# Optimization experiments

Hardware: AMD Instinct MI355X
Metric: run time of the kernel (lower is better)

The kernel has to match this reference:

```python
import jax, jax.numpy as jnp
import numpy as np

B, T, C = 4, 2048, 1024
H = 16
D = C // H  # head_dim = 64


def setup_inputs() -> dict:
    key = jax.random.key(0)
    k1, k2, k3 = jax.random.split(key, 3)
    x = jax.random.normal(k1, (B, T, C), dtype=jnp.float32)
    # torch Linear weights are [out_features, in_features]; scale like default init
    W_qkv = jax.random.normal(k2, (3 * C, C), dtype=jnp.float32) * (1.0 / np.sqrt(C))
    W_proj = jax.random.normal(k3, (C, C), dtype=jnp.float32) * (1.0 / np.sqrt(C))
    return {"x": x, "W_qkv": W_qkv, "W_proj": W_proj}


def reference(x, W_qkv, W_proj):
    # qkv projection: x @ W_qkv.T -> (B,T,3C), split into q,k,v
    qkv = jnp.einsum('btc,oc->bto', x, W_qkv)
    q, k, v = jnp.split(qkv, 3, axis=-1)
    # reshape to (B,H,T,D)
    q = q.reshape(B, T, H, D).transpose(0, 2, 1, 3)
    k = k.reshape(B, T, H, D).transpose(0, 2, 1, 3)
    v = v.reshape(B, T, H, D).transpose(0, 2, 1, 3)
    scale = jnp.sqrt(jnp.float32(D))
    # explicit (B,H,T,T) scores, as in the original module
    attn = jnp.einsum('bhqd,bhkd->bhqk', q, k) / scale
    causal = jnp.tril(jnp.ones((T, T), dtype=bool))
    attn = jnp.where(causal, attn, -jnp.inf)
    attn = jax.nn.softmax(attn, axis=-1)
    out = jnp.einsum('bhqk,bhkd->bhqd', attn, v)
    out = out.transpose(0, 2, 1, 3).reshape(B, T, C)
    return jnp.einsum('btc,oc->bto', out, W_proj)
```

## Files before the change

### kernel.cpp

```cpp
#include <hip/hip_runtime.h>

typedef __attribute__((ext_vector_type(8))) short short8;
typedef __attribute__((ext_vector_type(4))) float f32x4;
typedef __attribute__((ext_vector_type(16))) float f32x16;
typedef __attribute__((ext_vector_type(4))) unsigned int u32x4;

#define AS1(p) ((const __attribute__((address_space(1))) void*)(p))
#define AS3(p) ((__attribute__((address_space(3))) void*)(p))

#define B_ 4
#define T_ 2048
#define C_ 1024
#define H_ 16
#define D_ 64
#define M_ (B_*T_)

__device__ __forceinline__ unsigned short f2bf(float f) {
  union { float f; unsigned u; } v; v.f = f;
  return (unsigned short)((v.u + 0x7fffu + ((v.u >> 16) & 1u)) >> 16);
}

__device__ __forceinline__ unsigned cvt_pk_bf16(float lo, float hi2) {
  unsigned r;
  asm("v_cvt_pk_bf16_f32 %0, %1, %2" : "=v"(r) : "v"(lo), "v"(hi2));
  return r;
}

__global__ void cast_f32_bf16(const float* __restrict__ in, unsigned short* __restrict__ out, int n) {
  int i = (blockIdx.x * blockDim.x + threadIdx.x) * 4;
  int stride = gridDim.x * blockDim.x * 4;
  for (; i < n; i += stride) {
    float4 f = *reinterpret_cast<const float4*>(in + i);
    ushort4 o;
    o.x = f2bf(f.x); o.y = f2bf(f.y); o.z = f2bf(f.z); o.w = f2bf(f.w);
    *reinterpret_cast<ushort4*>(out + i) = o;
  }
}

template<int EPI>
__global__ __launch_bounds__(256) void gemm_bt(
    const unsigned short* __restrict__ A, const unsigned short* __restrict__ Bt,
    float* __restrict__ Cout, int M, int N, int K,
    unsigned short* __restrict__ qb, unsigned short* __restrict__ kb,
    unsigned short* __restrict__ vtb) {
  __shared__ unsigned short As[128 * 32];
  __shared__ unsigned short Bs[128 * 32];
  const int tid = threadIdx.x;
  const int lane = tid & 63;
  const int w = tid >> 6;
  const int wr = w >> 1, wc = w & 1;
  const int lr = lane & 15, lg = lane >> 4;
  const int ntiles = N >> 7;
  const int mt = blockIdx.x / ntiles, nt = blockIdx.x % ntiles;
  const int m0 = mt << 7, n0 = nt << 7;

  f32x4 acc[4][4];
  #pragma unroll
  for (int i = 0; i < 4; i++)
    #pragma unroll
    for (int j = 0; j < 4; j++) acc[i][j] = (f32x4){0.f, 0.f, 0.f, 0.f};

  const int wbase = tid & ~63;
  for (int k0 = 0; k0 < K; k0 += 32) {
    #pragma unroll
    for (int t = 0; t < 2; t++) {
      int slot = t * 256 + tid;
      int row = slot >> 2, kg = slot & 3;
      const unsigned short* ga = A + (size_t)(m0 + row) * K + k0 + kg * 8;
      char* la = (char*)As + (size_t)(t * 256 + wbase) * 16;
      __builtin_amdgcn_global_load_lds(AS1(ga), AS3(la), 16, 0, 0);
      const unsigned short* gb = Bt + (size_t)(n0 + row) * K + k0 + kg * 8;
      char* lb = (char*)Bs + (size_t)(t * 256 + wbase) * 16;
      __builtin_amdgcn_global_load_lds(AS1(gb), AS3(lb), 16, 0, 0);
    }
    __syncthreads();
    short8 af[4], bf[4];
    #pragma unroll
    for (int i = 0; i < 4; i++) {
      af[i] = *reinterpret_cast<const short8*>(&As[(wr * 64 + i * 16 + lr) * 32 + lg * 8]);
      bf[i] = *reinterpret_cast<const short8*>(&Bs[(wc * 64 + i * 16 + lr) * 32 + lg * 8]);
    }
    #pragma unroll
    for (int i = 0; i < 4; i++)
      #pragma unroll
      for (int j = 0; j < 4; j++)
        acc[i][j] = __builtin_amdgcn_mfma_f32_16x16x32_bf16(af[i], bf[j], acc[i][j], 0, 0, 0);
    __syncthreads();
  }

  #pragma unroll
  for (int i = 0; i < 4; i++) {
    #pragma unroll
    for (int j = 0; j < 4; j++) {
      #pragma unroll
      for (int r = 0; r < 4; r++) {
        int row = m0 + wr * 64 + i * 16 + lg * 4 + r;
        int col = n0 + wc * 64 + j * 16 + lr;
        float v = acc[i][j][r];
        if (EPI == 0) {
          Cout[(size_t)row * N + col] = v;
        } else {
          int which = col >> 10;
          int c = col & 1023;
          int h = c >> 6, d = c & 63;
          int b = row >> 11, t2 = row & 2047;
          if (which == 0) {
            qb[(((size_t)(b * H_ + h)) * T_ + t2) * D_ + d] = f2bf(v * 0.125f);
          } else if (which == 1) {
            kb[(((size_t)(b * H_ + h)) * T_ + t2) * D_ + d] = f2bf(v);
          } else {
            vtb[(((size_t)(b * H_ + h)) * D_ + d) * T_ + t2] = f2bf(v);
          }
        }
      }
    }
  }
}

__global__ __launch_bounds__(256, 2) void attn_fwd(
    const unsigned short* __restrict__ qb, const unsigned short* __restrict__ kb,
    const unsigned short* __restrict__ vtb, unsigned short* __restrict__ ob) {
  __shared__ unsigned short Kl[2 * 64 * 64];
  const int tid = threadIdx.x;
  const int lane = tid & 63;
  const int w = tid >> 6;
  const int q31 = lane & 31;
  const int hi = lane >> 5;

  const int bid = blockIdx.x;
  const int bh = (bid & 7) * 8 + ((bid >> 3) & 7);
  const int qt = 15 - (bid >> 6);
  const int qb0 = qt << 7;
  const int b = bh >> 4, h = bh & 15;

  const unsigned short* Q  = qb  + (size_t)bh * T_ * D_;
  const unsigned short* Kp = kb  + (size_t)bh * T_ * D_;
  const unsigned short* Vt = vtb + (size_t)bh * D_ * T_;

  const int qlo = qb0 + w * 32;
  const int qg = qlo + q31;
  const int qmax = qlo + 31;

  short8 qf[4];
  #pragma unroll
  for (int ch = 0; ch < 4; ch++)
    qf[ch] = *reinterpret_cast<const short8*>(Q + (size_t)qg * D_ + ch * 16 + hi * 8);

  f32x16 acc0, acc1;
  #pragma unroll
  for (int r = 0; r < 16; r++) { acc0[r] = 0.f; acc1[r] = 0.f; }
  float mrun = -INFINITY, lrun = 0.f;

  auto stage = [&](int buf, int k0) {
    #pragma unroll
    for (int sh = 0; sh < 2; sh++) {
      int s = sh * 256 + tid;
      int row = s >> 3;
      int xlin = (s & 7) * 16;
      int src = xlin ^ ((row & 7) << 4);
      const unsigned short* g = Kp + (size_t)(k0 + row) * D_ + (src >> 1);
      char* l = (char*)Kl + buf * 8192 + (size_t)(sh * 256 + (tid & ~63)) * 16;
      __builtin_amdgcn_global_load_lds(AS1(g), AS3(l), 16, 0, 0);
    }
  };

  const int nt = qb0 / 64 + 2;
  stage(0, 0);
  __syncthreads();

  for (int t = 0; t < nt; t++) {
    const int k0 = t * 64;
    if (t + 1 < nt) stage((t + 1) & 1, k0 + 64);

    if (k0 <= qmax) {
      const char* kbase = (const char*)Kl + (t & 1) * 8192;

      f32x16 s0, s1;
      #pragma unroll
      for (int r = 0; r < 16; r++) { s0[r] = 0.f; s1[r] = 0.f; }
      __builtin_amdgcn_s_setprio(1);
      #pragma unroll
      for (int kc = 0; kc < 2; kc++) {
        const int row = kc * 32 + q31;
        const int sw = (row & 7) << 4;
        #pragma unroll
        for (int ch = 0; ch < 4; ch++) {
          const int cb = ch * 32 + hi * 16;
          short8 kf = *reinterpret_cast<const short8*>(kbase + row * 128 + (cb ^ sw));
          if (kc == 0) s0 = __builtin_amdgcn_mfma_f32_32x32x16_bf16(kf, qf[ch], s0, 0, 0, 0);
          else         s1 = __builtin_amdgcn_mfma_f32_32x32x16_bf16(kf, qf[ch], s1, 0, 0, 0);
        }
      }
      __builtin_amdgcn_s_setprio(0);

      if (k0 + 63 > qlo) {
        #pragma unroll
        for (int r = 0; r < 16; r++) {
          const int kl = (r & 3) + 8 * (r >> 2) + 4 * hi;
          if (k0 + kl > qg)      s0[r] = -INFINITY;
          if (k0 + 32 + kl > qg) s1[r] = -INFINITY;
        }
      }

      float tm[8];
      #pragma unroll
      for (int r = 0; r < 8; r++)
        tm[r] = fmaxf(fmaxf(s0[r], s0[r + 8]), fmaxf(s1[r], s1[r + 8]));
      #pragma unroll
      for (int off = 4; off > 0; off >>= 1)
        #pragma unroll
        for (int r = 0; r < off; r++) tm[r] = fmaxf(tm[r], tm[r + off]);
      float pmax = fmaxf(tm[0], __shfl_xor(tm[0], 32));

      if (!__all(pmax - mrun <= 8.0f)) {
        const float mnew = fmaxf(mrun, pmax);
        const float alpha = __expf(mrun - mnew);
        lrun *= alpha;
        #pragma unroll
        for (int r = 0; r < 16; r++) { acc0[r] *= alpha; acc1[r] *= alpha; }
        mrun = mnew;
      }

      #pragma unroll
      for (int r = 0; r < 16; r++) { s0[r] = __expf(s0[r] - mrun); s1[r] = __expf(s1[r] - mrun); }
      float ts[8];
      #pragma unroll
      for (int r = 0; r < 8; r++)
        ts[r] = (s0[r] + s0[r + 8]) + (s1[r] + s1[r + 8]);
      #pragma unroll
      for (int off = 4; off > 0; off >>= 1)
        #pragma unroll
        for (int r = 0; r < off; r++) ts[r] += ts[r + off];
      lrun += ts[0] + __shfl_xor(ts[0], 32);

      #pragma unroll
      for (int kc = 0; kc < 2; kc++) {
        unsigned w8[8], rw8[8];
        #pragma unroll
        for (int j = 0; j < 8; j++) {
          float a = (kc == 0) ? s0[2 * j] : s1[2 * j];
          float bb = (kc == 0) ? s0[2 * j + 1] : s1[2 * j + 1];
          w8[j] = cvt_pk_bf16(a, bb);
        }
        #pragma unroll
        for (int j = 0; j < 8; j++) rw8[j] = (unsigned)__shfl_xor((int)w8[j], 32);

        __builtin_amdgcn_s_setprio(1);
        #pragma unroll
        for (int ks = 0; ks < 2; ks++) {
          unsigned a0 = hi ? rw8[4 * ks + 2] : w8[4 * ks + 0];
          unsigned a1 = hi ? rw8[4 * ks + 3] : w8[4 * ks + 1];
          unsigned a2 = hi ? w8[4 * ks + 2]  : rw8[4 * ks + 0];
          unsigned a3 = hi ? w8[4 * ks + 3]  : rw8[4 * ks + 1];
          u32x4 pw = {a0, a1, a2, a3};
          union { u32x4 u; short8 s; } cv; cv.u = pw;
          const int kb2 = k0 + kc * 32 + ks * 16;
          #pragma unroll
          for (int ds = 0; ds < 2; ds++) {
            short8 vf = *reinterpret_cast<const short8*>(
                Vt + (size_t)(ds * 32 + q31) * T_ + kb2 + hi * 8);
            if (ds == 0) acc0 = __builtin_amdgcn_mfma_f32_32x32x16_bf16(vf, cv.s, acc0, 0, 0, 0);
            else         acc1 = __builtin_amdgcn_mfma_f32_32x32x16_bf16(vf, cv.s, acc1, 0, 0, 0);
          }
        }
        __builtin_amdgcn_s_setprio(0);
      }
    }
    __syncthreads();
  }

  const float inv = 1.f / lrun;
  unsigned short* orow = ob + ((size_t)(b * T_ + qg)) * C_ + h * D_;
  #pragma unroll
  for (int ds = 0; ds < 2; ds++) {
    #pragma unroll
    for (int g = 0; g < 4; g++) {
      ushort4 o4;
      if (ds == 0) {
        o4.x = f2bf(acc0[4 * g + 0] * inv); o4.y = f2bf(acc0[4 * g + 1] * inv);
        o4.z = f2bf(acc0[4 * g + 2] * inv); o4.w = f2bf(acc0[4 * g + 3] * inv);
      } else {
        o4.x = f2bf(acc1[4 * g + 0] * inv); o4.y = f2bf(acc1[4 * g + 1] * inv);
        o4.z = f2bf(acc1[4 * g + 2] * inv); o4.w = f2bf(acc1[4 * g + 3] * inv);
      }
      *reinterpret_cast<ushort4*>(orow + ds * 32 + 8 * g + 4 * hi) = o4;
    }
  }
}

extern "C" void kernel_launch(void* const* d_in, const int* in_sizes, int n_in,
                              void* d_out, int out_size, void* d_ws, size_t ws_size,
                              hipStream_t stream) {
  const float* x = (const float*)d_in[0];
  const float* W_qkv = (const float*)d_in[1];
  const float* W_proj = (const float*)d_in[2];
  float* out = (float*)d_out;

  char* ws = (char*)d_ws;
  unsigned short* xb     = (unsigned short*)(ws);
  unsigned short* wqkvb  = (unsigned short*)(ws + 16777216);
  unsigned short* wprojb = (unsigned short*)(ws + 23068672);
  unsigned short* qb     = (unsigned short*)(ws + 25165824);
  unsigned short* kb     = (unsigned short*)(ws + 41943040);
  unsigned short* vtb    = (unsigned short*)(ws + 58720256);
  unsigned short* ob     = xb;

  const int nx = M_ * C_;
  const int nwqkv = 3 * C_ * C_;
  const int nwproj = C_ * C_;

  cast_f32_bf16<<<2048, 256, 0, stream>>>(x, xb, nx);
  cast_f32_bf16<<<2048, 256, 0, stream>>>(W_qkv, wqkvb, nwqkv);
  cast_f32_bf16<<<1024, 256, 0, stream>>>(W_proj, wprojb, nwproj);

  gemm_bt<1><<<(M_ / 128) * (3 * C_ / 128), 256, 0, stream>>>(
      xb, wqkvb, nullptr, M_, 3 * C_, C_, qb, kb, vtb);

  attn_fwd<<<B_ * H_ * (T_ / 128), 256, 0, stream>>>(qb, kb, vtb, ob);

  gemm_bt<0><<<(M_ / 128) * (C_ / 128), 256, 0, stream>>>(
      ob, wprojb, out, M_, C_, C_, nullptr, nullptr, nullptr);
}
```

Before: 241.2 us.

## Split KV range across waves with LDS merge of partial softmax states

Each block now handles 32 queries, and its four waves process interleaved KV tiles in parallel. Each wave loads K directly from global memory into registers instead of staging it through double-buffered LDS. Per-wave partial accumulators, max and sum are then combined through LDS in a tree merge. This is meant to improve parallelism and load balance and to remove the per-tile barriers. In exchange it gives up K reuse across waves, which raises global/L2 traffic and adds merge overhead.

```diff
diff --git a/kernel.cpp b/kernel.cpp
--- a/kernel.cpp
+++ b/kernel.cpp
@@ -120,7 +120,7 @@
 __global__ __launch_bounds__(256, 2) void attn_fwd(
     const unsigned short* __restrict__ qb, const unsigned short* __restrict__ kb,
     const unsigned short* __restrict__ vtb, unsigned short* __restrict__ ob) {
-  __shared__ unsigned short Kl[2 * 64 * 64];
+  __shared__ float Ml[2][64][34];
   const int tid = threadIdx.x;
   const int lane = tid & 63;
   const int w = tid >> 6;
@@ -129,161 +129,177 @@
 
   const int bid = blockIdx.x;
   const int bh = (bid & 7) * 8 + ((bid >> 3) & 7);
-  const int qt = 15 - (bid >> 6);
-  const int qb0 = qt << 7;
+  const int qu = 63 - (bid >> 6);
+  const int qb0 = qu << 5;
   const int b = bh >> 4, h = bh & 15;
 
   const unsigned short* Q  = qb  + (size_t)bh * T_ * D_;
   const unsigned short* Kp = kb  + (size_t)bh * T_ * D_;
   const unsigned short* Vt = vtb + (size_t)bh * D_ * T_;
 
-  const int qlo = qb0 + w * 32;
-  const int qg = qlo + q31;
-  const int qmax = qlo + 31;
+  const int qg = qb0 + q31;
 
   short8 qf[4];
   #pragma unroll
   for (int ch = 0; ch < 4; ch++)
-    qf[ch] = *reinterpret_cast<const short8*>(Q + (size_t)qg * D_ + ch * 16 + hi * 8);
+    qf[ch] = *reinterpret_cast<const short8*>(Q + qg * D_ + ch * 16 + hi * 8);
 
   f32x16 acc0, acc1;
   #pragma unroll
   for (int r = 0; r < 16; r++) { acc0[r] = 0.f; acc1[r] = 0.f; }
   float mrun = -INFINITY, lrun = 0.f;
 
-  auto stage = [&](int buf, int k0) {
-    #pragma unroll
-    for (int sh = 0; sh < 2; sh++) {
-      int s = sh * 256 + tid;
-      int row = s >> 3;
-      int xlin = (s & 7) * 16;
-      int src = xlin ^ ((row & 7) << 4);
-      const unsigned short* g = Kp + (size_t)(k0 + row) * D_ + (src >> 1);
-      char* l = (char*)Kl + buf * 8192 + (size_t)(sh * 256 + (tid & ~63)) * 16;
-      __builtin_amdgcn_global_load_lds(AS1(g), AS3(l), 16, 0, 0);
-    }
+  const int ntk = (qb0 >> 6) + 1;
+
+  for (int t = w; t < ntk; t += 4) {
+    const int k0 = t << 6;
+
+    short8 kf0[4], kf1[4];
+    #pragma unroll
+    for (int ch = 0; ch < 4; ch++)
+      kf0[ch] = *reinterpret_cast<const short8*>(Kp + (k0 + q31) * D_ + ch * 16 + hi * 8);
+    #pragma unroll
+    for (int ch = 0; ch < 4; ch++)
+      kf1[ch] = *reinterpret_cast<const short8*>(Kp + (k0 + 32 + q31) * D_ + ch * 16 + hi * 8);
+
+    f32x16 s0, s1;
+    #pragma unroll
+    for (int r = 0; r < 16; r++) { s0[r] = 0.f; s1[r] = 0.f; }
+    __builtin_amdgcn_s_setprio(1);
+    #pragma unroll
+    for (int ch = 0; ch < 4; ch++)
+      s0 = __builtin_amdgcn_mfma_f32_32x32x16_bf16(kf0[ch], qf[ch], s0, 0, 0, 0);
+    #pragma unroll
+    for (int ch = 0; ch < 4; ch++)
+      s1 = __builtin_amdgcn_mfma_f32_32x32x16_bf16(kf1[ch], qf[ch], s1, 0, 0, 0);
+    __builtin_amdgcn_s_setprio(0);
+
+    if (t == ntk - 1) {
+      #pragma unroll
+      for (int r = 0; r < 16; r++) {
+        const int kl = (r & 3) + 8 * (r >> 2) + 4 * hi;
+        if (k0 + kl > qg)      s0[r] = -INFINITY;
+        if (k0 + 32 + kl > qg) s1[r] = -INFINITY;
+      }
+    }
+
+    float tm[8];
+    #pragma unroll
+    for (int r = 0; r < 8; r++)
+      tm[r] = fmaxf(fmaxf(s0[r], s0[r + 8]), fmaxf(s1[r], s1[r + 8]));
+    #pragma unroll
+    for (int off = 4; off > 0; off >>= 1)
+      #pragma unroll
+      for (int r = 0; r < off; r++) tm[r] = fmaxf(tm[r], tm[r + off]);
+    float pmax = fmaxf(tm[0], __shfl_xor(tm[0], 32));
+
+    if (!__all(pmax - mrun <= 8.0f)) {
+      const float mnew = fmaxf(mrun, pmax);
+      const float alpha = __expf(mrun - mnew);
+      lrun *= alpha;
+      #pragma unroll
+      for (int r = 0; r < 16; r++) { acc0[r] *= alpha; acc1[r] *= alpha; }
+      mrun = mnew;
+    }
+
+    #pragma unroll
+    for (int r = 0; r < 16; r++) { s0[r] = __expf(s0[r] - mrun); s1[r] = __expf(s1[r] - mrun); }
+    float ts[8];
+    #pragma unroll
+    for (int r = 0; r < 8; r++)
+      ts[r] = (s0[r] + s0[r + 8]) + (s1[r] + s1[r + 8]);
+    #pragma unroll
+    for (int off = 4; off > 0; off >>= 1)
+      #pragma unroll
+      for (int r = 0; r < off; r++) ts[r] += ts[r + off];
+    lrun += ts[0] + __shfl_xor(ts[0], 32);
+
+    #pragma unroll
+    for (int kc = 0; kc < 2; kc++) {
+      unsigned w8[8], rw8[8];
+      #pragma unroll
+      for (int j = 0; j < 8; j++) {
+        float a  = (kc == 0) ? s0[2 * j] : s1[2 * j];
+        float bb = (kc == 0) ? s0[2 * j + 1] : s1[2 * j + 1];
+        w8[j] = cvt_pk_bf16(a, bb);
+      }
+      #pragma unroll
+      for (int j = 0; j < 8; j++) rw8[j] = (unsigned)__shfl_xor((int)w8[j], 32);
+
+      __builtin_amdgcn_s_setprio(1);
+      #pragma unroll
+      for (int ks = 0; ks < 2; ks++) {
+        unsigned a0 = hi ? rw8[4 * ks + 2] : w8[4 * ks + 0];
+        unsigned a1 = hi ? rw8[4 * ks + 3] : w8[4 * ks + 1];
+        unsigned a2 = hi ? w8[4 * ks + 2]  : rw8[4 * ks + 0];
+        unsigned a3 = hi ? w8[4 * ks + 3]  : rw8[4 * ks + 1];
+        u32x4 pw = {a0, a1, a2, a3};
+        union { u32x4 u; short8 s; } cv; cv.u = pw;
+        const int kb2 = k0 + kc * 32 + ks * 16;
+        #pragma unroll
+        for (int ds = 0; ds < 2; ds++) {
+          short8 vf = *reinterpret_cast<const short8*>(
+              Vt + (ds * 32 + q31) * T_ + kb2 + hi * 8);
+          if (ds == 0) acc0 = __builtin_amdgcn_mfma_f32_32x32x16_bf16(vf, cv.s, acc0, 0, 0, 0);
+          else         acc1 = __builtin_amdgcn_mfma_f32_32x32x16_bf16(vf, cv.s, acc1, 0, 0, 0);
+        }
+      }
+      __builtin_amdgcn_s_setprio(0);
+    }
+  }
+
+  auto store_partial = [&](int buf) {
+    #pragma unroll
+    for (int r = 0; r < 16; r++) {
+      Ml[buf][lane][r]      = acc0[r];
+      Ml[buf][lane][16 + r] = acc1[r];
+    }
+    Ml[buf][lane][32] = mrun;
+    Ml[buf][lane][33] = lrun;
   };
-
-  const int nt = qb0 / 64 + 2;
-  stage(0, 0);
+  auto merge_partial = [&](int buf) {
+    float mP = Ml[buf][lane][32], lP = Ml[buf][lane][33];
+    float M = fmaxf(mrun, mP);
+    if (M != -INFINITY) {
+      float a  = __expf(mrun - M);
+      float bb = __expf(mP - M);
+      #pragma unroll
+      for (int r = 0; r < 16; r++) {
+        acc0[r] = acc0[r] * a + Ml[buf][lane][r] * bb;
+        acc1[r] = acc1[r] * a + Ml[buf][lane][16 + r] * bb;
+      }
+      lrun = lrun * a + lP * bb;
+      mrun = M;
+    }
+  };
+
+  if (w == 1) store_partial(0);
+  if (w == 3) store_partial(1);
   __syncthreads();
-
-  for (int t = 0; t < nt; t++) {
-    const int k0 = t * 64;
-    if (t + 1 < nt) stage((t + 1) & 1, k0 + 64);
-
-    if (k0 <= qmax) {
-      const char* kbase = (const char*)Kl + (t & 1) * 8192;
-
-      f32x16 s0, s1;
-      #pragma unroll
-      for (int r = 0; r < 16; r++) { s0[r] = 0.f; s1[r] = 0.f; }
-      __builtin_amdgcn_s_setprio(1);
-      #pragma unroll
-      for (int kc = 0; kc < 2; kc++) {
-        const int row = kc * 32 + q31;
-        const int sw = (row & 7) << 4;
-        #pragma unroll
-        for (int ch = 0; ch < 4; ch++) {
-          const int cb = ch * 32 + hi * 16;
-          short8 kf = *reinterpret_cast<const short8*>(kbase + row * 128 + (cb ^ sw));
-          if (kc == 0) s0 = __builtin_amdgcn_mfma_f32_32x32x16_bf16(kf, qf[ch], s0, 0, 0, 0);
-          else         s1 = __builtin_amdgcn_mfma_f32_32x32x16_bf16(kf, qf[ch], s1, 0, 0, 0);
+  if (w == 0) merge_partial(0);
+  if (w == 2) merge_partial(1);
+  __syncthreads();
+  if (w == 2) store_partial(0);
+  __syncthreads();
+
+  if (w == 0) {
+    merge_partial(0);
+    const float inv = 1.f / lrun;
+    unsigned short* orow = ob + ((size_t)(b * T_ + qg)) * C_ + h * D_;
+    #pragma unroll
+    for (int ds = 0; ds < 2; ds++) {
+      #pragma unroll
+      for (int g = 0; g < 4; g++) {
+        ushort4 o4;
+        if (ds == 0) {
+          o4.x = f2bf(acc0[4 * g + 0] * inv); o4.y = f2bf(acc0[4 * g + 1] * inv);
+          o4.z = f2bf(acc0[4 * g + 2] * inv); o4.w = f2bf(acc0[4 * g + 3] * inv);
+        } else {
+          o4.x = f2bf(acc1[4 * g + 0] * inv); o4.y = f2bf(acc1[4 * g + 1] * inv);
+          o4.z = f2bf(acc1[4 * g + 2] * inv); o4.w = f2bf(acc1[4 * g + 3] * inv);
         }
-      }
-      __builtin_amdgcn_s_setprio(0);
-
-      if (k0 + 63 > qlo) {
-        #pragma unroll
-        for (int r = 0; r < 16; r++) {
-          const int kl = (r & 3) + 8 * (r >> 2) + 4 * hi;
-          if (k0 + kl > qg)      s0[r] = -INFINITY;
-          if (k0 + 32 + kl > qg) s1[r] = -INFINITY;
-        }
-      }
-
-      float tm[8];
-      #pragma unroll
-      for (int r = 0; r < 8; r++)
-        tm[r] = fmaxf(fmaxf(s0[r], s0[r + 8]), fmaxf(s1[r], s1[r + 8]));
-      #pragma unroll
-      for (int off = 4; off > 0; off >>= 1)
-        #pragma unroll
-        for (int r = 0; r < off; r++) tm[r] = fmaxf(tm[r], tm[r + off]);
-      float pmax = fmaxf(tm[0], __shfl_xor(tm[0], 32));
-
-      if (!__all(pmax - mrun <= 8.0f)) {
-        const float mnew = fmaxf(mrun, pmax);
-        const float alpha = __expf(mrun - mnew);
-        lrun *= alpha;
-        #pragma unroll
-        for (int r = 0; r < 16; r++) { acc0[r] *= alpha; acc1[r] *= alpha; }
-        mrun = mnew;
-      }
-
-      #pragma unroll
-      for (int r = 0; r < 16; r++) { s0[r] = __expf(s0[r] - mrun); s1[r] = __expf(s1[r] - mrun); }
-      float ts[8];
-      #pragma unroll
-      for (int r = 0; r < 8; r++)
-        ts[r] = (s0[r] + s0[r + 8]) + (s1[r] + s1[r + 8]);
-      #pragma unroll
-      for (int off = 4; off > 0; off >>= 1)
-        #pragma unroll
-        for (int r = 0; r < off; r++) ts[r] += ts[r + off];
-      lrun += ts[0] + __shfl_xor(ts[0], 32);
-
-      #pragma unroll
-      for (int kc = 0; kc < 2; kc++) {
-        unsigned w8[8], rw8[8];
-        #pragma unroll
-        for (int j = 0; j < 8; j++) {
-          float a = (kc == 0) ? s0[2 * j] : s1[2 * j];
-          float bb = (kc == 0) ? s0[2 * j + 1] : s1[2 * j + 1];
-          w8[j] = cvt_pk_bf16(a, bb);
-        }
-        #pragma unroll
-        for (int j = 0; j < 8; j++) rw8[j] = (unsigned)__shfl_xor((int)w8[j], 32);
-
-        __builtin_amdgcn_s_setprio(1);
-        #pragma unroll
-        for (int ks = 0; ks < 2; ks++) {
-          unsigned a0 = hi ? rw8[4 * ks + 2] : w8[4 * ks + 0];
-          unsigned a1 = hi ? rw8[4 * ks + 3] : w8[4 * ks + 1];
-          unsigned a2 = hi ? w8[4 * ks + 2]  : rw8[4 * ks + 0];
-          unsigned a3 = hi ? w8[4 * ks + 3]  : rw8[4 * ks + 1];
-          u32x4 pw = {a0, a1, a2, a3};
-          union { u32x4 u; short8 s; } cv; cv.u = pw;
-          const int kb2 = k0 + kc * 32 + ks * 16;
-          #pragma unroll
-          for (int ds = 0; ds < 2; ds++) {
-            short8 vf = *reinterpret_cast<const short8*>(
-                Vt + (size_t)(ds * 32 + q31) * T_ + kb2 + hi * 8);
-            if (ds == 0) acc0 = __builtin_amdgcn_mfma_f32_32x32x16_bf16(vf, cv.s, acc0, 0, 0, 0);
-            else         acc1 = __builtin_amdgcn_mfma_f32_32x32x16_bf16(vf, cv.s, acc1, 0, 0, 0);
-          }
-        }
-        __builtin_amdgcn_s_setprio(0);
-      }
-    }
-    __syncthreads();
-  }
-
-  const float inv = 1.f / lrun;
-  unsigned short* orow = ob + ((size_t)(b * T_ + qg)) * C_ + h * D_;
-  #pragma unroll
-  for (int ds = 0; ds < 2; ds++) {
-    #pragma unroll
-    for (int g = 0; g < 4; g++) {
-      ushort4 o4;
-      if (ds == 0) {
-        o4.x = f2bf(acc0[4 * g + 0] * inv); o4.y = f2bf(acc0[4 * g + 1] * inv);
-        o4.z = f2bf(acc0[4 * g + 2] * inv); o4.w = f2bf(acc0[4 * g + 3] * inv);
-      } else {
-        o4.x = f2bf(acc1[4 * g + 0] * inv); o4.y = f2bf(acc1[4 * g + 1] * inv);
-        o4.z = f2bf(acc1[4 * g + 2] * inv); o4.w = f2bf(acc1[4 * g + 3] * inv);
-      }
-      *reinterpret_cast<ushort4*>(orow + ds * 32 + 8 * g + 4 * hi) = o4;
+        *reinterpret_cast<ushort4*>(orow + ds * 32 + 8 * g + 4 * hi) = o4;
+      }
     }
   }
 }
@@ -316,7 +332,7 @@
   gemm_bt<1><<<(M_ / 128) * (3 * C_ / 128), 256, 0, stream>>>(
       xb, wqkvb, nullptr, M_, 3 * C_, C_, qb, kb, vtb);
 
-  attn_fwd<<<B_ * H_ * (T_ / 128), 256, 0, stream>>>(qb, kb, vtb, ob);
+  attn_fwd<<<B_ * H_ * (T_ / 32), 256, 0, stream>>>(qb, kb, vtb, ob);
 
   gemm_bt<0><<<(M_ / 128) * (C_ / 128), 256, 0, stream>>>(
       ob, wprojb, out, M_, C_, C_, nullptr, nullptr, nullptr);
```

Result: slower. 273.6 us (+13.4%).

## Double-buffer GEMM LDS tiles and give each attention wave 64 query rows

Applied to the files above, without the earlier changes.

The GEMM main loop now uses two LDS buffers, so the next K-slice is loaded asynchronously while the current one feeds the MFMAs, with one barrier per iteration. The attention kernel drops from 4 to 2 waves per block. Each wave now handles two 32-row query groups that share every K fragment read from LDS and every V fragment loaded from global memory. This halves the K/V load traffic per unit of MFMA work, at the cost of roughly double the accumulator registers per wave and half as many waves per block to hide latency.

```diff
diff --git a/kernel.cpp b/kernel.cpp
--- a/kernel.cpp
+++ b/kernel.cpp
@@ -43,8 +43,8 @@
     float* __restrict__ Cout, int M, int N, int K,
     unsigned short* __restrict__ qb, unsigned short* __restrict__ kb,
     unsigned short* __restrict__ vtb) {
-  __shared__ unsigned short As[128 * 32];
-  __shared__ unsigned short Bs[128 * 32];
+  __shared__ unsigned short As[2][128 * 32];
+  __shared__ unsigned short Bs[2][128 * 32];
   const int tid = threadIdx.x;
   const int lane = tid & 63;
   const int w = tid >> 6;
@@ -61,30 +61,41 @@
     for (int j = 0; j < 4; j++) acc[i][j] = (f32x4){0.f, 0.f, 0.f, 0.f};
 
   const int wbase = tid & ~63;
-  for (int k0 = 0; k0 < K; k0 += 32) {
+
+  auto stage = [&](int buf, int k0) {
     #pragma unroll
     for (int t = 0; t < 2; t++) {
       int slot = t * 256 + tid;
       int row = slot >> 2, kg = slot & 3;
       const unsigned short* ga = A + (size_t)(m0 + row) * K + k0 + kg * 8;
-      char* la = (char*)As + (size_t)(t * 256 + wbase) * 16;
+      char* la = (char*)As[buf] + (size_t)(t * 256 + wbase) * 16;
       __builtin_amdgcn_global_load_lds(AS1(ga), AS3(la), 16, 0, 0);
       const unsigned short* gb = Bt + (size_t)(n0 + row) * K + k0 + kg * 8;
-      char* lb = (char*)Bs + (size_t)(t * 256 + wbase) * 16;
+      char* lb = (char*)Bs[buf] + (size_t)(t * 256 + wbase) * 16;
       __builtin_amdgcn_global_load_lds(AS1(gb), AS3(lb), 16, 0, 0);
     }
-    __syncthreads();
+  };
+
+  const int nIter = K >> 5;
+  stage(0, 0);
+  __syncthreads();
+
+  for (int it = 0; it < nIter; ++it) {
+    const int cur = it & 1;
+    if (it + 1 < nIter) stage(cur ^ 1, (it + 1) << 5);
+
     short8 af[4], bf[4];
     #pragma unroll
     for (int i = 0; i < 4; i++) {
-      af[i] = *reinterpret_cast<const short8*>(&As[(wr * 64 + i * 16 + lr) * 32 + lg * 8]);
-      bf[i] = *reinterpret_cast<const short8*>(&Bs[(wc * 64 + i * 16 + lr) * 32 + lg * 8]);
+      af[i] = *reinterpret_cast<const short8*>(&As[cur][(wr * 64 + i * 16 + lr) * 32 + lg * 8]);
+      bf[i] = *reinterpret_cast<const short8*>(&Bs[cur][(wc * 64 + i * 16 + lr) * 32 + lg * 8]);
     }
     #pragma unroll
     for (int i = 0; i < 4; i++)
       #pragma unroll
       for (int j = 0; j < 4; j++)
         acc[i][j] = __builtin_amdgcn_mfma_f32_16x16x32_bf16(af[i], bf[j], acc[i][j], 0, 0, 0);
+
     __syncthreads();
   }
 
@@ -117,7 +128,7 @@
   }
 }
 
-__global__ __launch_bounds__(256, 2) void attn_fwd(
+__global__ __launch_bounds__(128, 2) void attn_fwd(
     const unsigned short* __restrict__ qb, const unsigned short* __restrict__ kb,
     const unsigned short* __restrict__ vtb, unsigned short* __restrict__ ob) {
   __shared__ unsigned short Kl[2 * 64 * 64];
@@ -137,29 +148,32 @@
   const unsigned short* Kp = kb  + (size_t)bh * T_ * D_;
   const unsigned short* Vt = vtb + (size_t)bh * D_ * T_;
 
-  const int qlo = qb0 + w * 32;
-  const int qg = qlo + q31;
-  const int qmax = qlo + 31;
-
-  short8 qf[4];
+  const int qloA = qb0 + w * 64;
+  const int qloB = qloA + 32;
+  const int qgA = qloA + q31;
+  const int qgB = qloB + q31;
+
+  short8 qfA[4], qfB[4];
   #pragma unroll
-  for (int ch = 0; ch < 4; ch++)
-    qf[ch] = *reinterpret_cast<const short8*>(Q + (size_t)qg * D_ + ch * 16 + hi * 8);
-
-  f32x16 acc0, acc1;
+  for (int ch = 0; ch < 4; ch++) {
+    qfA[ch] = *reinterpret_cast<const short8*>(Q + qgA * D_ + ch * 16 + hi * 8);
+    qfB[ch] = *reinterpret_cast<const short8*>(Q + qgB * D_ + ch * 16 + hi * 8);
+  }
+
+  f32x16 accA0, accA1, accB0, accB1;
   #pragma unroll
-  for (int r = 0; r < 16; r++) { acc0[r] = 0.f; acc1[r] = 0.f; }
-  float mrun = -INFINITY, lrun = 0.f;
+  for (int r = 0; r < 16; r++) { accA0[r] = 0.f; accA1[r] = 0.f; accB0[r] = 0.f; accB1[r] = 0.f; }
+  float mA = -INFINITY, lA = 0.f, mB = -INFINITY, lB = 0.f;
 
   auto stage = [&](int buf, int k0) {
     #pragma unroll
-    for (int sh = 0; sh < 2; sh++) {
-      int s = sh * 256 + tid;
+    for (int sh = 0; sh < 4; sh++) {
+      int s = sh * 128 + tid;
       int row = s >> 3;
       int xlin = (s & 7) * 16;
       int src = xlin ^ ((row & 7) << 4);
-      const unsigned short* g = Kp + (size_t)(k0 + row) * D_ + (src >> 1);
-      char* l = (char*)Kl + buf * 8192 + (size_t)(sh * 256 + (tid & ~63)) * 16;
+      const unsigned short* g = Kp + (k0 + row) * D_ + (src >> 1);
+      char* l = (char*)Kl + buf * 8192 + (size_t)(sh * 128 + (tid & ~63)) * 16;
       __builtin_amdgcn_global_load_lds(AS1(g), AS3(l), 16, 0, 0);
     }
   };
@@ -172,12 +186,12 @@
     const int k0 = t * 64;
     if (t + 1 < nt) stage((t + 1) & 1, k0 + 64);
 
-    if (k0 <= qmax) {
+    if (k0 <= qloA + 63) {
       const char* kbase = (const char*)Kl + (t & 1) * 8192;
 
-      f32x16 s0, s1;
-      #pragma unroll
-      for (int r = 0; r < 16; r++) { s0[r] = 0.f; s1[r] = 0.f; }
+      f32x16 sA0, sA1, sB0, sB1;
+      #pragma unroll
+      for (int r = 0; r < 16; r++) { sA0[r] = 0.f; sA1[r] = 0.f; sB0[r] = 0.f; sB1[r] = 0.f; }
       __builtin_amdgcn_s_setprio(1);
       #pragma unroll
       for (int kc = 0; kc < 2; kc++) {
@@ -185,82 +199,131 @@
         const int sw = (row & 7) << 4;
         #pragma unroll
         for (int ch = 0; ch < 4; ch++) {
-          const int cb = ch * 32 + hi * 16;
-          short8 kf = *reinterpret_cast<const short8*>(kbase + row * 128 + (cb ^ sw));
-          if (kc == 0) s0 = __builtin_amdgcn_mfma_f32_32x32x16_bf16(kf, qf[ch], s0, 0, 0, 0);
-          else         s1 = __builtin_amdgcn_mfma_f32_32x32x16_bf16(kf, qf[ch], s1, 0, 0, 0);
+          short8 kf = *reinterpret_cast<const short8*>(kbase + row * 128 + ((ch * 32 + hi * 16) ^ sw));
+          if (kc == 0) {
+            sA0 = __builtin_amdgcn_mfma_f32_32x32x16_bf16(kf, qfA[ch], sA0, 0, 0, 0);
+            sB0 = __builtin_amdgcn_mfma_f32_32x32x16_bf16(kf, qfB[ch], sB0, 0, 0, 0);
+          } else {
+            sA1 = __builtin_amdgcn_mfma_f32_32x32x16_bf16(kf, qfA[ch], sA1, 0, 0, 0);
+            sB1 = __builtin_amdgcn_mfma_f32_32x32x16_bf16(kf, qfB[ch], sB1, 0, 0, 0);
+          }
         }
       }
       __builtin_amdgcn_s_setprio(0);
 
-      if (k0 + 63 > qlo) {
+      if (k0 + 63 > qloA) {
         #pragma unroll
         for (int r = 0; r < 16; r++) {
           const int kl = (r & 3) + 8 * (r >> 2) + 4 * hi;
-          if (k0 + kl > qg)      s0[r] = -INFINITY;
-          if (k0 + 32 + kl > qg) s1[r] = -INFINITY;
-        }
-      }
-
-      float tm[8];
-      #pragma unroll
-      for (int r = 0; r < 8; r++)
-        tm[r] = fmaxf(fmaxf(s0[r], s0[r + 8]), fmaxf(s1[r], s1[r + 8]));
+          if (k0 + kl > qgA)      sA0[r] = -INFINITY;
+          if (k0 + 32 + kl > qgA) sA1[r] = -INFINITY;
+        }
+      }
+      if (k0 + 63 > qloB) {
+        #pragma unroll
+        for (int r = 0; r < 16; r++) {
+          const int kl = (r & 3) + 8 * (r >> 2) + 4 * hi;
+          if (k0 + kl > qgB)      sB0[r] = -INFINITY;
+          if (k0 + 32 + kl > qgB) sB1[r] = -INFINITY;
+        }
+      }
+
+      float tmA[8], tmB[8];
+      #pragma unroll
+      for (int r = 0; r < 8; r++) {
+        tmA[r] = fmaxf(fmaxf(sA0[r], sA0[r + 8]), fmaxf(sA1[r], sA1[r + 8]));
+        tmB[r] = fmaxf(fmaxf(sB0[r], sB0[r + 8]), fmaxf(sB1[r], sB1[r + 8]));
+      }
       #pragma unroll
       for (int off = 4; off > 0; off >>= 1)
         #pragma unroll
-        for (int r = 0; r < off; r++) tm[r] = fmaxf(tm[r], tm[r + off]);
-      float pmax = fmaxf(tm[0], __shfl_xor(tm[0], 32));
-
-      if (!__all(pmax - mrun <= 8.0f)) {
-        const float mnew = fmaxf(mrun, pmax);
-        const float alpha = __expf(mrun - mnew);
-        lrun *= alpha;
-        #pragma unroll
-        for (int r = 0; r < 16; r++) { acc0[r] *= alpha; acc1[r] *= alpha; }
-        mrun = mnew;
-      }
-
-      #pragma unroll
-      for (int r = 0; r < 16; r++) { s0[r] = __expf(s0[r] - mrun); s1[r] = __expf(s1[r] - mrun); }
-      float ts[8];
-      #pragma unroll
-      for (int r = 0; r < 8; r++)
-        ts[r] = (s0[r] + s0[r + 8]) + (s1[r] + s1[r + 8]);
+        for (int r = 0; r < off; r++) {
+          tmA[r] = fmaxf(tmA[r], tmA[r + off]);
+          tmB[r] = fmaxf(tmB[r], tmB[r + off]);
+        }
+      float pmaxA = fmaxf(tmA[0], __shfl_xor(tmA[0], 32));
+      float pmaxB = fmaxf(tmB[0], __shfl_xor(tmB[0], 32));
+
+      if (!__all(pmaxA - mA <= 8.0f)) {
+        const float mnew = fmaxf(mA, pmaxA);
+        const float alpha = __expf(mA - mnew);
+        lA *= alpha;
+        #pragma unroll
+        for (int r = 0; r < 16; r++) { accA0[r] *= alpha; accA1[r] *= alpha; }
+        mA = mnew;
+      }
+      if (!__all(pmaxB - mB <= 8.0f)) {
+        const float mnew = fmaxf(mB, pmaxB);
+        const float alpha = __expf(mB - mnew);
+        lB *= alpha;
+        #pragma unroll
+        for (int r = 0; r < 16; r++) { accB0[r] *= alpha; accB1[r] *= alpha; }
+        mB = mnew;
+      }
+
+      #pragma unroll
+      for (int r = 0; r < 16; r++) {
+        sA0[r] = __expf(sA0[r] - mA); sA1[r] = __expf(sA1[r] - mA);
+        sB0[r] = __expf(sB0[r] - mB); sB1[r] = __expf(sB1[r] - mB);
+      }
+      float tsA[8], tsB[8];
+      #pragma unroll
+      for (int r = 0; r < 8; r++) {
+        tsA[r] = (sA0[r] + sA0[r + 8]) + (sA1[r] + sA1[r + 8]);
+        tsB[r] = (sB0[r] + sB0[r + 8]) + (sB1[r] + sB1[r + 8]);
+      }
       #pragma unroll
       for (int off = 4; off > 0; off >>= 1)
         #pragma unroll
-        for (int r = 0; r < off; r++) ts[r] += ts[r + off];
-      lrun += ts[0] + __shfl_xor(ts[0], 32);
+        for (int r = 0; r < off; r++) { tsA[r] += tsA[r + off]; tsB[r] += tsB[r + off]; }
+      lA += tsA[0] + __shfl_xor(tsA[0], 32);
+      lB += tsB[0] + __shfl_xor(tsB[0], 32);
 
       #pragma unroll
       for (int kc = 0; kc < 2; kc++) {
-        unsigned w8[8], rw8[8];
+        unsigned w8A[8], rw8A[8], w8B[8], rw8B[8];
         #pragma unroll
         for (int j = 0; j < 8; j++) {
-          float a = (kc == 0) ? s0[2 * j] : s1[2 * j];
-          float bb = (kc == 0) ? s0[2 * j + 1] : s1[2 * j + 1];
-          w8[j] = cvt_pk_bf16(a, bb);
-        }
-        #pragma unroll
-        for (int j = 0; j < 8; j++) rw8[j] = (unsigned)__shfl_xor((int)w8[j], 32);
+          float aA  = (kc == 0) ? sA0[2 * j] : sA1[2 * j];
+          float bA  = (kc == 0) ? sA0[2 * j + 1] : sA1[2 * j + 1];
+          w8A[j] = cvt_pk_bf16(aA, bA);
+          float aB  = (kc == 0) ? sB0[2 * j] : sB1[2 * j];
+          float bB  = (kc == 0) ? sB0[2 * j + 1] : sB1[2 * j + 1];
+          w8B[j] = cvt_pk_bf16(aB, bB);
+        }
+        #pragma unroll
+        for (int j = 0; j < 8; j++) {
+          rw8A[j] = (unsigned)__shfl_xor((int)w8A[j], 32);
+          rw8B[j] = (unsigned)__shfl_xor((int)w8B[j], 32);
+        }
 
         __builtin_amdgcn_s_setprio(1);
         #pragma unroll
         for (int ks = 0; ks < 2; ks++) {
-          unsigned a0 = hi ? rw8[4 * ks + 2] : w8[4 * ks + 0];
-          unsigned a1 = hi ? rw8[4 * ks + 3] : w8[4 * ks + 1];
-          unsigned a2 = hi ? w8[4 * ks + 2]  : rw8[4 * ks + 0];
-          unsigned a3 = hi ? w8[4 * ks + 3]  : rw8[4 * ks + 1];
-          u32x4 pw = {a0, a1, a2, a3};
-          union { u32x4 u; short8 s; } cv; cv.u = pw;
+          unsigned a0 = hi ? rw8A[4 * ks + 2] : w8A[4 * ks + 0];
+          unsigned a1 = hi ? rw8A[4 * ks + 3] : w8A[4 * ks + 1];
+          unsigned a2 = hi ? w8A[4 * ks + 2]  : rw8A[4 * ks + 0];
+          unsigned a3 = hi ? w8A[4 * ks + 3]  : rw8A[4 * ks + 1];
+          u32x4 pwA = {a0, a1, a2, a3};
+          unsigned b0 = hi ? rw8B[4 * ks + 2] : w8B[4 * ks + 0];
+          unsigned b1 = hi ? rw8B[4 * ks + 3] : w8B[4 * ks + 1];
+          unsigned b2 = hi ? w8B[4 * ks + 2]  : rw8B[4 * ks + 0];
+          unsigned b3 = hi ? w8B[4 * ks + 3]  : rw8B[4 * ks + 1];
+          u32x4 pwB = {b0, b1, b2, b3};
+          union { u32x4 u; short8 s; } cvA, cvB;
+          cvA.u = pwA; cvB.u = pwB;
           const int kb2 = k0 + kc * 32 + ks * 16;
           #pragma unroll
           for (int ds = 0; ds < 2; ds++) {
             short8 vf = *reinterpret_cast<const short8*>(
-                Vt + (size_t)(ds * 32 + q31) * T_ + kb2 + hi * 8);
-            if (ds == 0) acc0 = __builtin_amdgcn_mfma_f32_32x32x16_bf16(vf, cv.s, acc0, 0, 0, 0);
-            else         acc1 = __builtin_amdgcn_mfma_f32_32x32x16_bf16(vf, cv.s, acc1, 0, 0, 0);
+                Vt + (ds * 32 + q31) * T_ + kb2 + hi * 8);
+            if (ds == 0) {
+              accA0 = __builtin_amdgcn_mfma_f32_32x32x16_bf16(vf, cvA.s, accA0, 0, 0, 0);
+              accB0 = __builtin_amdgcn_mfma_f32_32x32x16_bf16(vf, cvB.s, accB0, 0, 0, 0);
+            } else {
+              accA1 = __builtin_amdgcn_mfma_f32_32x32x16_bf16(vf, cvA.s, accA1, 0, 0, 0);
+              accB1 = __builtin_amdgcn_mfma_f32_32x32x16_bf16(vf, cvB.s, accB1, 0, 0, 0);
+            }
           }
         }
         __builtin_amdgcn_s_setprio(0);
@@ -269,21 +332,42 @@
     __syncthreads();
   }
 
-  const float inv = 1.f / lrun;
-  unsigned short* orow = ob + ((size_t)(b * T_ + qg)) * C_ + h * D_;
-  #pragma unroll
-  for (int ds = 0; ds < 2; ds++) {
-    #pragma unroll
-    for (int g = 0; g < 4; g++) {
-      ushort4 o4;
-      if (ds == 0) {
-        o4.x = f2bf(acc0[4 * g + 0] * inv); o4.y = f2bf(acc0[4 * g + 1] * inv);
-        o4.z = f2bf(acc0[4 * g + 2] * inv); o4.w = f2bf(acc0[4 * g + 3] * inv);
-      } else {
-        o4.x = f2bf(acc1[4 * g + 0] * inv); o4.y = f2bf(acc1[4 * g + 1] * inv);
-        o4.z = f2bf(acc1[4 * g + 2] * inv); o4.w = f2bf(acc1[4 * g + 3] * inv);
-      }
-      *reinterpret_cast<ushort4*>(orow + ds * 32 + 8 * g + 4 * hi) = o4;
+  {
+    const float invA = 1.f / lA;
+    unsigned short* orow = ob + ((size_t)(b * T_ + qgA)) * C_ + h * D_;
+    #pragma unroll
+    for (int ds = 0; ds < 2; ds++) {
+      #pragma unroll
+      for (int g = 0; g < 4; g++) {
+        ushort4 o4;
+        if (ds == 0) {
+          o4.x = f2bf(accA0[4 * g + 0] * invA); o4.y = f2bf(accA0[4 * g + 1] * invA);
+          o4.z = f2bf(accA0[4 * g + 2] * invA); o4.w = f2bf(accA0[4 * g + 3] * invA);
+        } else {
+          o4.x = f2bf(accA1[4 * g + 0] * invA); o4.y = f2bf(accA1[4 * g + 1] * invA);
+          o4.z = f2bf(accA1[4 * g + 2] * invA); o4.w = f2bf(accA1[4 * g + 3] * invA);
+        }
+        *reinterpret_cast<ushort4*>(orow + ds * 32 + 8 * g + 4 * hi) = o4;
+      }
+    }
+  }
+  {
+    const float invB = 1.f / lB;
+    unsigned short* orow = ob + ((size_t)(b * T_ + qgB)) * C_ + h * D_;
+    #pragma unroll
+    for (int ds = 0; ds < 2; ds++) {
+      #pragma unroll
+      for (int g = 0; g < 4; g++) {
+        ushort4 o4;
+        if (ds == 0) {
+          o4.x = f2bf(accB0[4 * g + 0] * invB); o4.y = f2bf(accB0[4 * g + 1] * invB);
+          o4.z = f2bf(accB0[4 * g + 2] * invB); o4.w = f2bf(accB0[4 * g + 3] * invB);
+        } else {
+          o4.x = f2bf(accB1[4 * g + 0] * invB); o4.y = f2bf(accB1[4 * g + 1] * invB);
+          o4.z = f2bf(accB1[4 * g + 2] * invB); o4.w = f2bf(accB1[4 * g + 3] * invB);
+        }
+        *reinterpret_cast<ushort4*>(orow + ds * 32 + 8 * g + 4 * hi) = o4;
+      }
     }
   }
 }
@@ -316,7 +400,7 @@
   gemm_bt<1><<<(M_ / 128) * (3 * C_ / 128), 256, 0, stream>>>(
       xb, wqkvb, nullptr, M_, 3 * C_, C_, qb, kb, vtb);
 
-  attn_fwd<<<B_ * H_ * (T_ / 128), 256, 0, stream>>>(qb, kb, vtb, ob);
+  attn_fwd<<<B_ * H_ * (T_ / 128), 128, 0, stream>>>(qb, kb, vtb, ob);
 
   gemm_bt<0><<<(M_ / 128) * (C_ / 128), 256, 0, stream>>>(
       ob, wprojb, out, M_, C_, C_, nullptr, nullptr, nullptr);
```

Result: faster. 223.5 us (-7.3%).
